# Optimization experiments

Measured on AMD Instinct MI355X. Metric: run time of the kernel, lower is better.

Reference implementation:

```python
import jax, jax.numpy as jnp
import numpy as np

D_MODEL = 256
D_STATE = 2
BATCH = 8
SEQ = 8192


def setup_inputs() -> dict:
    key = jax.random.key(0)
    ks = jax.random.split(key, 8)
    s = 1.0 / np.sqrt(D_STATE)
    x = jax.random.normal(ks[0], (BATCH, SEQ, D_MODEL), dtype=jnp.float32)
    # stable range so exp(cumsum) stays finite at T=8192 (see notes)
    log_a_mag = -jax.random.uniform(ks[1], (D_MODEL, D_STATE), jnp.float32, 1e-5, 1e-3)
    a_phase = jax.random.uniform(ks[2], (D_MODEL, D_STATE), jnp.float32, 0.0, 2.0 * np.pi)
    B_re = jax.random.normal(ks[3], (D_MODEL, D_STATE), jnp.float32) * s
    B_im = jax.random.normal(ks[4], (D_MODEL, D_STATE), jnp.float32) * s
    C_re = jax.random.normal(ks[5], (D_MODEL, D_STATE), jnp.float32) * s
    C_im = jax.random.normal(ks[6], (D_MODEL, D_STATE), jnp.float32) * s
    D_diag = jnp.ones((D_MODEL,), jnp.float32)
    return dict(x=x, log_a_mag=log_a_mag, a_phase=a_phase, B_re=B_re, B_im=B_im,
                C_re=C_re, C_im=C_im, D_diag=D_diag)


def reference(x, log_a_mag, a_phase, B_re, B_im, C_re, C_im, D_diag):
    # x: (B, T, D); params: (D, S)
    Bsz, T, D = x.shape
    S = log_a_mag.shape[1]
    # cumulative complex log-decay along time, shape (D, S, T)
    cum_r = jnp.cumsum(jnp.broadcast_to(log_a_mag[:, :, None], (D, S, T)), axis=-1)
    cum_i = jnp.cumsum(jnp.broadcast_to(a_phase[:, :, None], (D, S, T)), axis=-1)
    x_t = jnp.swapaxes(x, 1, 2)                      # (B, D, T)
    Bu_r = B_re[None, :, :, None] * x_t[:, :, None, :]   # (B, D, S, T)
    Bu_i = B_im[None, :, :, None] * x_t[:, :, None, :]
    # exp(-cum_log_a): descale inputs
    en = jnp.exp(-cum_r)
    enr = en * jnp.cos(-cum_i)
    eni = en * jnp.sin(-cum_i)
    sr = enr * Bu_r - eni * Bu_i
    si = enr * Bu_i + eni * Bu_r
    csr = jnp.cumsum(sr, axis=-1)
    csi = jnp.cumsum(si, axis=-1)
    # exp(+cum_log_a): rescale prefix sums -> hidden states h (B, D, S, T)
    ec = jnp.exp(cum_r)
    ecr = ec * jnp.cos(cum_i)
    eci = ec * jnp.sin(cum_i)
    h_r = ecr * csr - eci * csi
    h_i = ecr * csi + eci * csr
    # output: Re(C . h) summed over state + skip D*x
    y = jnp.einsum('bdst,ds->bdt', h_r, C_re) - jnp.einsum('bdst,ds->bdt', h_i, C_im)
    y = jnp.swapaxes(y, 1, 2) + D_diag * x           # (B, T, D)
    return y
```

## Files before the change

### kernel.cpp

```cpp
#include <hip/hip_runtime.h>
#include <math.h>

#define BATCH  8
#define SEQ    8192
#define DMODEL 256
#define DSTATE 2
#define CHUNKS 256
#define CLEN   32


__global__ void ssm_chunk_state(const float* __restrict__ x,
                                const float* __restrict__ lam,
                                const float* __restrict__ aph,
                                const float* __restrict__ Bre,
                                const float* __restrict__ Bim,
                                float* __restrict__ E) {
    const int lane = threadIdx.x;
    const int bid  = blockIdx.x;
    const int b = bid / CHUNKS;
    const int c = bid % CHUNKS;
    const int d0 = lane * 4;

    float ar[4][2], ai[4][2], br[4][2], bi[4][2];
#pragma unroll
    for (int j = 0; j < 4; ++j) {
        const int d = d0 + j;
#pragma unroll
        for (int s = 0; s < 2; ++s) {
            const float lm = lam[d * 2 + s];
            const float ph = aph[d * 2 + s];
            const float m  = expf(lm);
            ar[j][s] = m * cosf(ph);
            ai[j][s] = m * sinf(ph);
            br[j][s] = Bre[d * 2 + s];
            bi[j][s] = Bim[d * 2 + s];
        }
    }

    float hr[4][2] = {}, hi[4][2] = {};

    const float* xp = x + ((size_t)b * SEQ + (size_t)c * CLEN) * DMODEL + d0;
#pragma unroll 4
    for (int t = 0; t < CLEN; ++t) {
        const float4 xv = *reinterpret_cast<const float4*>(xp + (size_t)t * DMODEL);
        const float xj[4] = {xv.x, xv.y, xv.z, xv.w};
#pragma unroll
        for (int j = 0; j < 4; ++j) {
#pragma unroll
            for (int s = 0; s < 2; ++s) {
                const float nr = fmaf(ar[j][s], hr[j][s],
                                 fmaf(-ai[j][s], hi[j][s], br[j][s] * xj[j]));
                const float ni = fmaf(ar[j][s], hi[j][s],
                                 fmaf( ai[j][s], hr[j][s], bi[j][s] * xj[j]));
                hr[j][s] = nr;
                hi[j][s] = ni;
            }
        }
    }

    float* ep = E + ((size_t)(b * CHUNKS + c) * 64 + lane) * 16;
#pragma unroll
    for (int j = 0; j < 4; ++j) {
        float4 v;
        v.x = hr[j][0]; v.y = hi[j][0];
        v.z = hr[j][1]; v.w = hi[j][1];
        reinterpret_cast<float4*>(ep)[j] = v;
    }
}

__global__ void ssm_chunk_scan(const float* __restrict__ E,
                               float* __restrict__ Hin,
                               const float* __restrict__ lam,
                               const float* __restrict__ aph) {
    const int lane = threadIdx.x & 63;
    const int g = blockIdx.x * 4 + (threadIdx.x >> 6);
    const int b = g >> 9;
    const int r = g & 511;
    const int d = (r >> 3) * 4 + ((r >> 1) & 3);
    const int s = r & 1;

    const double lm = (double)lam[d * 2 + s];
    const double ph = (double)aph[d * 2 + s];
    {
    }
    const double mL = exp(lm * (double)CLEN);
    const double pL = ph * (double)CLEN;
    const float Ar = (float)(mL * cos(pL));
    const float Ai = (float)(mL * sin(pL));

    const size_t base = (size_t)b * CHUNKS * 1024 + (size_t)r * 2;

    float2 e[4];
#pragma unroll
    for (int i = 0; i < 4; ++i) {
        const int c = lane * 4 + i;
        e[i] = *reinterpret_cast<const float2*>(E + base + (size_t)c * 1024);
    }

    float vr = e[0].x, vi = e[0].y;
#pragma unroll
    for (int i = 1; i < 4; ++i) {
        const float nr = fmaf(Ar, vr, fmaf(-Ai, vi, e[i].x));
        const float ni = fmaf(Ar, vi, fmaf( Ai, vr, e[i].y));
        vr = nr; vi = ni;
    }

#pragma unroll
    for (int st = 0; st < 6; ++st) {
        const int k = 1 << st;
        const double n = (double)CLEN * 4.0 * (double)k;
        const double mm = exp(lm * n);
        const double pp = ph * n;
        const float Wr = (float)(mm * cos(pp));
        const float Wi = (float)(mm * sin(pp));
        const float ur = __shfl_up(vr, (unsigned)k);
        const float ui = __shfl_up(vi, (unsigned)k);
        if (lane >= k) {
            vr = fmaf(Wr, ur, fmaf(-Wi, ui, vr));
            vi = fmaf(Wr, ui, fmaf( Wi, ur, vi));
        }
    }

    float pr = __shfl_up(vr, 1);
    float pi = __shfl_up(vi, 1);
    if (lane == 0) { pr = 0.f; pi = 0.f; }

#pragma unroll
    for (int i = 0; i < 4; ++i) {
        const int c = lane * 4 + i;
        *reinterpret_cast<float2*>(Hin + base + (size_t)c * 1024) = make_float2(pr, pi);
        const float nr = fmaf(Ar, pr, fmaf(-Ai, pi, e[i].x));
        const float ni = fmaf(Ar, pi, fmaf( Ai, pr, e[i].y));
        pr = nr; pi = ni;
    }
}

__global__ void ssm_output(const float* __restrict__ x,
                           const float* __restrict__ lam,
                           const float* __restrict__ aph,
                           const float* __restrict__ Bre,
                           const float* __restrict__ Bim,
                           const float* __restrict__ Cre,
                           const float* __restrict__ Cim,
                           const float* __restrict__ Dd,
                           const float* __restrict__ Hin,
                           float* __restrict__ y) {
    const int lane = threadIdx.x;
    const int bid  = blockIdx.x;
    const int b = bid / CHUNKS;
    const int c = bid % CHUNKS;
    const int d0 = lane * 4;

    float ar[4][2], ai[4][2], br[4][2], bi[4][2], cr[4][2], ci[4][2], dd[4];
#pragma unroll
    for (int j = 0; j < 4; ++j) {
        const int d = d0 + j;
        dd[j] = Dd[d];
#pragma unroll
        for (int s = 0; s < 2; ++s) {
            const float lm = lam[d * 2 + s];
            const float ph = aph[d * 2 + s];
            const float m  = expf(lm);
            ar[j][s] = m * cosf(ph);
            ai[j][s] = m * sinf(ph);
            br[j][s] = Bre[d * 2 + s];
            bi[j][s] = Bim[d * 2 + s];
            cr[j][s] = Cre[d * 2 + s];
            ci[j][s] = Cim[d * 2 + s];
        }
    }

    float hr[4][2], hi[4][2];
    const float* hp = Hin + ((size_t)(b * CHUNKS + c) * 64 + lane) * 16;
#pragma unroll
    for (int j = 0; j < 4; ++j) {
        const float4 v = reinterpret_cast<const float4*>(hp)[j];
        hr[j][0] = v.x; hi[j][0] = v.y;
        hr[j][1] = v.z; hi[j][1] = v.w;
    }

    const size_t tbase = ((size_t)b * SEQ + (size_t)c * CLEN) * DMODEL + d0;
    const float* xp = x + tbase;
    float* yp = y + tbase;
#pragma unroll 4
    for (int t = 0; t < CLEN; ++t) {
        const float4 xv = *reinterpret_cast<const float4*>(xp + (size_t)t * DMODEL);
        const float xj[4] = {xv.x, xv.y, xv.z, xv.w};
        float yj[4];
#pragma unroll
        for (int j = 0; j < 4; ++j) {
            float acc = dd[j] * xj[j];
#pragma unroll
            for (int s = 0; s < 2; ++s) {
                const float nr = fmaf(ar[j][s], hr[j][s],
                                 fmaf(-ai[j][s], hi[j][s], br[j][s] * xj[j]));
                const float ni = fmaf(ar[j][s], hi[j][s],
                                 fmaf( ai[j][s], hr[j][s], bi[j][s] * xj[j]));
                hr[j][s] = nr;
                hi[j][s] = ni;
                acc = fmaf(cr[j][s], nr, acc);
                acc = fmaf(-ci[j][s], ni, acc);
            }
            yj[j] = acc;
        }
        float4 yv;
        yv.x = yj[0]; yv.y = yj[1]; yv.z = yj[2]; yv.w = yj[3];
        *reinterpret_cast<float4*>(yp + (size_t)t * DMODEL) = yv;
    }
}

extern "C" void kernel_launch(void* const* d_in, const int* in_sizes, int n_in,
                              void* d_out, int out_size, void* d_ws, size_t ws_size,
                              hipStream_t stream) {
    const float* x   = (const float*)d_in[0];
    const float* lam = (const float*)d_in[1];
    const float* aph = (const float*)d_in[2];
    const float* Bre = (const float*)d_in[3];
    const float* Bim = (const float*)d_in[4];
    const float* Cre = (const float*)d_in[5];
    const float* Cim = (const float*)d_in[6];
    const float* Dd  = (const float*)d_in[7];
    float* y = (float*)d_out;

    float* E   = (float*)d_ws;
    float* Hin = E + (size_t)BATCH * CHUNKS * 1024;

    ssm_chunk_state<<<BATCH * CHUNKS, 64, 0, stream>>>(x, lam, aph, Bre, Bim, E);
    ssm_chunk_scan<<<(BATCH * 512) / 4, 256, 0, stream>>>(E, Hin, lam, aph);
    ssm_output<<<BATCH * CHUNKS, 64, 0, stream>>>(x, lam, aph, Bre, Bim, Cre, Cim, Dd, Hin, y);
}
```

Before: 170.3 us.

## Fuse three SSM chunk-scan kernels into one cooperative kernel with grid syncs

```diff
diff --git a/kernel.cpp b/kernel.cpp
--- a/kernel.cpp
+++ b/kernel.cpp
@@ -1,5 +1,8 @@
 #include <hip/hip_runtime.h>
+#include <hip/hip_cooperative_groups.h>
 #include <math.h>
+
+namespace cg = cooperative_groups;
 
 #define BATCH  8
 #define SEQ    8192
@@ -8,6 +11,189 @@
 #define CHUNKS 256
 #define CLEN   32
 
+
+__global__ void __launch_bounds__(256, 2)
+ssm_fused(const float* __restrict__ x,
+          const float* __restrict__ lam,
+          const float* __restrict__ aph,
+          const float* __restrict__ Bre,
+          const float* __restrict__ Bim,
+          const float* __restrict__ Cre,
+          const float* __restrict__ Cim,
+          const float* __restrict__ Dd,
+          float* __restrict__ E,
+          float* __restrict__ Hin,
+          float* __restrict__ y) {
+    const int lane = threadIdx.x & 63;
+    const int w = blockIdx.x * 4 + (threadIdx.x >> 6);
+    const int b = w >> 8;
+    const int c = w & (CHUNKS - 1);
+    const int d0 = lane * 4;
+
+    float ar[4][2], ai[4][2], br[4][2], bi[4][2];
+#pragma unroll
+    for (int j = 0; j < 4; ++j) {
+        const int d = d0 + j;
+#pragma unroll
+        for (int s = 0; s < 2; ++s) {
+            const float lm = lam[d * 2 + s];
+            const float ph = aph[d * 2 + s];
+            const float m  = expf(lm);
+            ar[j][s] = m * cosf(ph);
+            ai[j][s] = m * sinf(ph);
+            br[j][s] = Bre[d * 2 + s];
+            bi[j][s] = Bim[d * 2 + s];
+        }
+    }
+
+    const float* xp = x + ((size_t)b * SEQ + (size_t)c * CLEN) * DMODEL + d0;
+
+    {
+        float hr[4][2] = {}, hi[4][2] = {};
+#pragma unroll 4
+        for (int t = 0; t < CLEN; ++t) {
+            const float4 xv = *reinterpret_cast<const float4*>(xp + (size_t)t * DMODEL);
+            const float xj[4] = {xv.x, xv.y, xv.z, xv.w};
+#pragma unroll
+            for (int j = 0; j < 4; ++j) {
+#pragma unroll
+                for (int s = 0; s < 2; ++s) {
+                    const float nr = fmaf(ar[j][s], hr[j][s],
+                                     fmaf(-ai[j][s], hi[j][s], br[j][s] * xj[j]));
+                    const float ni = fmaf(ar[j][s], hi[j][s],
+                                     fmaf( ai[j][s], hr[j][s], bi[j][s] * xj[j]));
+                    hr[j][s] = nr;
+                    hi[j][s] = ni;
+                }
+            }
+        }
+        float* ep = E + ((size_t)w * 64 + lane) * 16;
+#pragma unroll
+        for (int j = 0; j < 4; ++j) {
+            float4 v;
+            v.x = hr[j][0]; v.y = hi[j][0];
+            v.z = hr[j][1]; v.w = hi[j][1];
+            reinterpret_cast<float4*>(ep)[j] = v;
+        }
+    }
+
+    __threadfence();
+    cg::this_grid().sync();
+
+#pragma unroll
+    for (int i = 0; i < 2; ++i) {
+        const int g = w * 2 + i;
+        const int sb = g >> 9;
+        const int r  = g & 511;
+        const int sd = (r >> 3) * 4 + ((r >> 1) & 3);
+        const int ss = r & 1;
+
+        const double lmD = (double)lam[sd * 2 + ss];
+        const double phD = (double)aph[sd * 2 + ss];
+        const double mL = exp(lmD * (double)CLEN);
+        const double pL = phD * (double)CLEN;
+        const float Ar = (float)(mL * cos(pL));
+        const float Ai = (float)(mL * sin(pL));
+
+        const size_t base = (size_t)sb * CHUNKS * 1024 + (size_t)r * 2;
+
+        float2 e[4];
+#pragma unroll
+        for (int k = 0; k < 4; ++k) {
+            const int cc = lane * 4 + k;
+            e[k] = *reinterpret_cast<const float2*>(E + base + (size_t)cc * 1024);
+        }
+
+        float vr = e[0].x, vi = e[0].y;
+#pragma unroll
+        for (int k = 1; k < 4; ++k) {
+            const float nr = fmaf(Ar, vr, fmaf(-Ai, vi, e[k].x));
+            const float ni = fmaf(Ar, vi, fmaf( Ai, vr, e[k].y));
+            vr = nr; vi = ni;
+        }
+
+#pragma unroll
+        for (int st = 0; st < 6; ++st) {
+            const int k = 1 << st;
+            const double n = (double)CLEN * 4.0 * (double)k;
+            const double mm = exp(lmD * n);
+            const double pp = phD * n;
+            const float Wr = (float)(mm * cos(pp));
+            const float Wi = (float)(mm * sin(pp));
+            const float ur = __shfl_up(vr, (unsigned)k);
+            const float ui = __shfl_up(vi, (unsigned)k);
+            if (lane >= k) {
+                vr = fmaf(Wr, ur, fmaf(-Wi, ui, vr));
+                vi = fmaf(Wr, ui, fmaf( Wi, ur, vi));
+            }
+        }
+
+        float pr = __shfl_up(vr, 1);
+        float pi = __shfl_up(vi, 1);
+        if (lane == 0) { pr = 0.f; pi = 0.f; }
+
+#pragma unroll
+        for (int k = 0; k < 4; ++k) {
+            const int cc = lane * 4 + k;
+            *reinterpret_cast<float2*>(Hin + base + (size_t)cc * 1024) =
+                make_float2(pr, pi);
+            const float nr = fmaf(Ar, pr, fmaf(-Ai, pi, e[k].x));
+            const float ni = fmaf(Ar, pi, fmaf( Ai, pr, e[k].y));
+            pr = nr; pi = ni;
+        }
+    }
+
+    __threadfence();
+    cg::this_grid().sync();
+
+    float cr[4][2], ci[4][2], dd[4];
+#pragma unroll
+    for (int j = 0; j < 4; ++j) {
+        const int d = d0 + j;
+        dd[j] = Dd[d];
+#pragma unroll
+        for (int s = 0; s < 2; ++s) {
+            cr[j][s] = Cre[d * 2 + s];
+            ci[j][s] = Cim[d * 2 + s];
+        }
+    }
+
+    float hr[4][2], hi[4][2];
+    const float* hp = Hin + ((size_t)w * 64 + lane) * 16;
+#pragma unroll
+    for (int j = 0; j < 4; ++j) {
+        const float4 v = reinterpret_cast<const float4*>(hp)[j];
+        hr[j][0] = v.x; hi[j][0] = v.y;
+        hr[j][1] = v.z; hi[j][1] = v.w;
+    }
+
+    float* yp = y + ((size_t)b * SEQ + (size_t)c * CLEN) * DMODEL + d0;
+#pragma unroll 4
+    for (int t = 0; t < CLEN; ++t) {
+        const float4 xv = *reinterpret_cast<const float4*>(xp + (size_t)t * DMODEL);
+        const float xj[4] = {xv.x, xv.y, xv.z, xv.w};
+        float yj[4];
+#pragma unroll
+        for (int j = 0; j < 4; ++j) {
+            float acc = dd[j] * xj[j];
+#pragma unroll
+            for (int s = 0; s < 2; ++s) {
+                const float nr = fmaf(ar[j][s], hr[j][s],
+                                 fmaf(-ai[j][s], hi[j][s], br[j][s] * xj[j]));
+                const float ni = fmaf(ar[j][s], hi[j][s],
+                                 fmaf( ai[j][s], hr[j][s], bi[j][s] * xj[j]));
+                hr[j][s] = nr;
+                hi[j][s] = ni;
+                acc = fmaf(cr[j][s], nr, acc);
+                acc = fmaf(-ci[j][s], ni, acc);
+            }
+            yj[j] = acc;
+        }
+        float4 yv;
+        yv.x = yj[0]; yv.y = yj[1]; yv.z = yj[2]; yv.w = yj[3];
+        *reinterpret_cast<float4*>(yp + (size_t)t * DMODEL) = yv;
+    }
+}
 
 __global__ void ssm_chunk_state(const float* __restrict__ x,
                                 const float* __restrict__ lam,
@@ -38,7 +224,6 @@
     }
 
     float hr[4][2] = {}, hi[4][2] = {};
-
     const float* xp = x + ((size_t)b * SEQ + (size_t)c * CLEN) * DMODEL + d0;
 #pragma unroll 4
     for (int t = 0; t < CLEN; ++t) {
@@ -81,8 +266,6 @@
 
     const double lm = (double)lam[d * 2 + s];
     const double ph = (double)aph[d * 2 + s];
-    {
-    }
     const double mL = exp(lm * (double)CLEN);
     const double pL = ph * (double)CLEN;
     const float Ar = (float)(mL * cos(pL));
@@ -92,10 +275,8 @@
 
     float2 e[4];
 #pragma unroll
-    for (int i = 0; i < 4; ++i) {
-        const int c = lane * 4 + i;
-        e[i] = *reinterpret_cast<const float2*>(E + base + (size_t)c * 1024);
-    }
+    for (int i = 0; i < 4; ++i)
+        e[i] = *reinterpret_cast<const float2*>(E + base + (size_t)(lane * 4 + i) * 1024);
 
     float vr = e[0].x, vi = e[0].y;
 #pragma unroll
@@ -127,8 +308,8 @@
 
 #pragma unroll
     for (int i = 0; i < 4; ++i) {
-        const int c = lane * 4 + i;
-        *reinterpret_cast<float2*>(Hin + base + (size_t)c * 1024) = make_float2(pr, pi);
+        *reinterpret_cast<float2*>(Hin + base + (size_t)(lane * 4 + i) * 1024) =
+            make_float2(pr, pi);
         const float nr = fmaf(Ar, pr, fmaf(-Ai, pi, e[i].x));
         const float ni = fmaf(Ar, pi, fmaf( Ai, pr, e[i].y));
         pr = nr; pi = ni;
@@ -220,12 +401,25 @@
     const float* Cre = (const float*)d_in[5];
     const float* Cim = (const float*)d_in[6];
     const float* Dd  = (const float*)d_in[7];
-    float* y = (float*)d_out;
+    float* yo = (float*)d_out;
 
     float* E   = (float*)d_ws;
     float* Hin = E + (size_t)BATCH * CHUNKS * 1024;
 
-    ssm_chunk_state<<<BATCH * CHUNKS, 64, 0, stream>>>(x, lam, aph, Bre, Bim, E);
-    ssm_chunk_scan<<<(BATCH * 512) / 4, 256, 0, stream>>>(E, Hin, lam, aph);
-    ssm_output<<<BATCH * CHUNKS, 64, 0, stream>>>(x, lam, aph, Bre, Bim, Cre, Cim, Dd, Hin, y);
+    void* args[] = {
+        (void*)&x, (void*)&lam, (void*)&aph, (void*)&Bre, (void*)&Bim,
+        (void*)&Cre, (void*)&Cim, (void*)&Dd, (void*)&E, (void*)&Hin,
+        (void*)&yo,
+    };
+    hipError_t err = hipLaunchCooperativeKernel(
+        reinterpret_cast<void*>(ssm_fused),
+        dim3(BATCH * CHUNKS / 4), dim3(256), args, 0, stream);
+
+    if (err != hipSuccess) {
+        (void)hipGetLastError();
+        ssm_chunk_state<<<BATCH * CHUNKS, 64, 0, stream>>>(x, lam, aph, Bre, Bim, E);
+        ssm_chunk_scan<<<(BATCH * 512) / 4, 256, 0, stream>>>(E, Hin, lam, aph);
+        ssm_output<<<BATCH * CHUNKS, 64, 0, stream>>>(x, lam, aph, Bre, Bim,
+                                                      Cre, Cim, Dd, Hin, yo);
+    }
 }
```

New measurement: 429.8 us. +152.4%, slower.
